# Kernel optimization log

Hardware: AMD Instinct MI355X
Metric: run time of the kernel (lower is better)

Reference implementation:

```python
import jax, jax.numpy as jnp
from jax import lax
import numpy as np

B, T, N, D = 16, 2048, 8, 512


def _div_term(d):
    # exp(arange(0,d,2) * -(ln 10000)/d), as in FixedEmbedding
    return jnp.exp(jnp.arange(0, d, 2).astype(jnp.float32) * (-np.log(10000.0) / d))


def _fixed_table(c, d):
    pos = jnp.arange(c, dtype=jnp.float32)[:, None]
    ang = pos * _div_term(d)  # [c, d/2]
    tab = jnp.zeros((c, d), dtype=jnp.float32)
    tab = tab.at[:, 0::2].set(jnp.sin(ang)).at[:, 1::2].set(jnp.cos(ang))
    return tab


def setup_inputs() -> dict:
    key = jax.random.key(0)
    k1, k2, k3 = jax.random.split(key, 3)
    x = jax.random.normal(k1, (B, T, N), dtype=jnp.float32)
    x_mark = jax.random.randint(k2, (B, T, 4), 0, 7).astype(jnp.int64)
    conv_w = jax.random.normal(k3, (D, N, 3), dtype=jnp.float32) * 0.05
    return {"x": x, "x_mark": x_mark, "conv_w": conv_w}


def reference(x, x_mark, conv_w):
    b, t, n = x.shape
    d = conv_w.shape[0]

    # --- TokenEmbedding: Conv1d(c_in->d_model, k=3, circular padding, no bias) ---
    xp = jnp.transpose(x, (0, 2, 1))  # [b, n, t]
    xpad = jnp.concatenate([xp[..., -1:], xp, xp[..., :1]], axis=-1)  # circular pad 1
    val = lax.conv_general_dilated(
        xpad, conv_w, window_strides=(1,), padding="VALID",
        dimension_numbers=("NCH", "OIH", "NCH"))  # [b, d, t]
    val = jnp.transpose(val, (0, 2, 1))  # [b, t, d]

    # --- TemporalEmbedding (fixed sinusoidal tables), freq='h' ---
    # columns: 0=month(<13), 1=day(<32), 2=weekday(<7), 3=hour(<24)
    temp = (_fixed_table(24, d)[x_mark[:, :, 3]]
            + _fixed_table(7, d)[x_mark[:, :, 2]]
            + _fixed_table(32, d)[x_mark[:, :, 1]]
            + _fixed_table(13, d)[x_mark[:, :, 0]])  # [b, t, d]

    # --- Cycle_PositionalEmbedding (k=1) ---
    fft_abs = jnp.abs(jnp.fft.rfft(x, axis=1))  # [b, t//2+1, n]
    top_idx = jnp.argmax(fft_abs, axis=1)  # [b, n]; topk(k=1) == argmax (first max)
    freqs = jnp.fft.fftfreq(t, d=1.0)  # length t; rfft indices are in range
    periods = jnp.clip(t / freqs[top_idx], 1.0, float(t))  # [b, n]; 0-freq -> inf -> t
    time_idx = jnp.arange(t, dtype=jnp.float32)[None, :, None]  # [1, t, 1]
    pidx = jnp.floor(time_idx % periods[:, None, :])  # [b, t, n] (.long() truncation)

    # FixedEmbedding row for index p is sin/cos(p*div) independent of c_in
    ang = pidx[..., None] * _div_term(d)  # [b, t, n, d/2]
    pe = jnp.stack([jnp.sin(ang), jnp.cos(ang)], axis=-1).reshape(b, t, n, d)
    cyc = pe.mean(axis=2)  # [b, t, d]

    # dropout is identity in eval mode
    return val + temp + cyc
```

## Files before the change

### kernel.cpp

```cpp
#include <hip/hip_runtime.h>
#include <math.h>

#define B_ 16
#define T_ 2048
#define N_ 8
#define D_ 512
#define DTW 4
#define LPAD 520

#define NEG_W0 (-3.0679615757712823e-3f)
#define NEG_W32 (-0.19634954084936207f)
#define NEG_W1024 (-6.1359231515425647e-3f)
#define NEG_LDIV (-0.035977892078031555f)

typedef __attribute__((ext_vector_type(8))) short bf16x8;
typedef __attribute__((ext_vector_type(4))) float f32x4;

static __device__ __forceinline__ short f2bf(float f) {
  unsigned int u = __float_as_uint(f);
  unsigned int r = u + 0x7FFFu + ((u >> 16) & 1u);
  return (short)(r >> 16);
}


__global__ __launch_bounds__(512) void prep_kernel(
    const float* __restrict__ x, const int* __restrict__ xmark,
    const float* __restrict__ convw, float* __restrict__ pmax,
    float* __restrict__ nyqS, float* __restrict__ tab,
    short* __restrict__ amat, short* __restrict__ xbf,
    short* __restrict__ cnt) {
  int tid = threadIdx.x;
  int blk = blockIdx.x;

  if (blk >= 512) {
    int j = blk - 512;
    if (j < 64) {
      int r = j * 512 + tid;
      const float4* xr = (const float4*)(x + (size_t)r * 8);
      float4 lo = xr[0], hi = xr[1];
      bf16x8 v;
      v[0] = f2bf(lo.x); v[1] = f2bf(lo.y); v[2] = f2bf(lo.z); v[3] = f2bf(lo.w);
      v[4] = f2bf(hi.x); v[5] = f2bf(hi.y); v[6] = f2bf(hi.z); v[7] = f2bf(hi.w);
      *(bf16x8*)(xbf + (size_t)r * 8) = v;
      int4 mk = *(const int4*)(xmark + (size_t)r * 4);
      bf16x8 cv;
#pragma unroll
      for (int p = 0; p < 8; ++p) {
        int cc = (mk.x == p) + (mk.y == p) + (mk.z == p) + (mk.w == p);
        cv[p] = f2bf((float)cc);
      }
      *(bf16x8*)(cnt + (size_t)r * 8) = cv;
    } else if (j == 64) {
      int d = tid;
      short row[32];
#pragma unroll
      for (int kk = 0; kk < 24; ++kk) {
        int g = kk >> 3, n = kk & 7;
        row[kk] = f2bf(convw[d * 24 + n * 3 + g]);
      }
      float divv = expf((float)(d >> 1) * NEG_LDIV);
      float s1, c1;
      sincosf(divv, &s1, &c1);
      int odd = d & 1;
      row[24] = f2bf(odd ? 1.f : 0.f);
      float ps = s1, pc = c1;
      row[25] = f2bf(odd ? pc : ps);
#pragma unroll
      for (int p = 2; p < 7; ++p) {
        float ns = fmaf(ps, c1, pc * s1);
        float nc = fmaf(pc, c1, -ps * s1);
        ps = ns; pc = nc;
        row[24 + p] = f2bf(odd ? pc : ps);
      }
      row[31] = 0;
#pragma unroll
      for (int q = 0; q < 4; ++q)
        *(bf16x8*)(amat + d * 32 + q * 8) = *(bf16x8*)&row[q * 8];
    } else {
      int gt = (j - 65) * 512 + tid;
      int tb = gt >> 7;
      int d4 = gt & 127;
      float dv0 = expf((float)(d4 * 2) * NEG_LDIV);
      float dv1 = expf((float)(d4 * 2 + 1) * NEG_LDIV);
      float tf = (float)(tb * 16);
      float s0, c0, s1, c1, r0s, r0c, r1s, r1c;
      sincosf(tf * dv0, &s0, &c0);
      sincosf(tf * dv1, &s1, &c1);
      sincosf(dv0, &r0s, &r0c);
      sincosf(dv1, &r1s, &r1c);
      float* row = tab + (size_t)(tb * 16) * D_ + d4 * 4;
#pragma unroll
      for (int u = 0; u < 16; ++u) {
        f32x4 v; v[0] = s0; v[1] = c0; v[2] = s1; v[3] = c1;
        *(f32x4*)row = v;
        row += D_;
        float ns0 = fmaf(s0, r0c, c0 * r0s), nc0 = fmaf(c0, r0c, -s0 * r0s);
        s0 = ns0; c0 = nc0;
        float ns1 = fmaf(s1, r1c, c1 * r1s), nc1 = fmaf(c1, r1c, -s1 * r1s);
        s1 = ns1; c1 = nc1;
      }
    }
    return;
  }

  __shared__ __align__(16) float2 ybuf[1024];
  __shared__ __align__(16) float2 Bl[1024];
  __shared__ __align__(16) float2 part[512];
  __shared__ float swav[8];
  __shared__ float pwav[4];
  int bn = blk >> 2;
  int parity = (blk >> 1) & 1;
  int h = blk & 1;
  int b = bn >> 3, n = bn & 7;
  const float* xb = x + (size_t)b * (T_ * N_) + n;

  float v0 = xb[tid * 8];
  float v1 = xb[(tid + 512) * 8];
  float v2 = xb[(tid + 1024) * 8];
  float v3 = xb[(tid + 1536) * 8];
  float ea = v0 + v2, eb = v1 + v3;
  float sgn = (tid & 1) ? -(ea + eb) : (ea + eb);
#pragma unroll
  for (int off = 32; off > 0; off >>= 1) sgn += __shfl_down(sgn, off);
  if ((tid & 63) == 0) swav[tid >> 6] = sgn;

  if (parity == 0) {
    float* ya = (float*)ybuf;
    ya[tid] = ea;
    ya[tid + 512] = eb;
  } else {
    float oa = v0 - v2, ob = v1 - v3;
    float ca, sa, cb, sb;
    sincosf((float)tid * NEG_W0, &sa, &ca);
    sincosf((float)(tid + 512) * NEG_W0, &sb, &cb);
    ybuf[tid] = make_float2(oa * ca, oa * sa);
    ybuf[tid + 512] = make_float2(ob * cb, ob * sb);
  }
  __syncthreads();

  int m0 = tid & 31, t0a = tid >> 5;
  float d1 = (float)m0 * NEG_W32;
  float K1 = 2.0f * cosf(d1);
  float c = 1.f, s = 0.f, cp, sp;
  sincosf(-d1, &sp, &cp);
  float ar0 = 0.f, ai0 = 0.f, ar1 = 0.f, ai1 = 0.f;
  if (parity == 0) {
    const float* ya = (const float*)ybuf;
#pragma unroll 8
    for (int t1 = 0; t1 < 32; ++t1) {
      float y0 = ya[t1 * 32 + t0a];
      float y1 = ya[t1 * 32 + t0a + 16];
      ar0 = fmaf(y0, c, ar0); ai0 = fmaf(y0, s, ai0);
      ar1 = fmaf(y1, c, ar1); ai1 = fmaf(y1, s, ai1);
      float nc = fmaf(K1, c, -cp), ns = fmaf(K1, s, -sp);
      cp = c; sp = s; c = nc; s = ns;
    }
  } else {
#pragma unroll 8
    for (int t1 = 0; t1 < 32; ++t1) {
      float2 y0 = ybuf[t1 * 32 + t0a];
      float2 y1 = ybuf[t1 * 32 + t0a + 16];
      ar0 = fmaf(y0.x, c, fmaf(-y0.y, s, ar0));
      ai0 = fmaf(y0.x, s, fmaf(y0.y, c, ai0));
      ar1 = fmaf(y1.x, c, fmaf(-y1.y, s, ar1));
      ai1 = fmaf(y1.x, s, fmaf(y1.y, c, ai1));
      float nc = fmaf(K1, c, -cp), ns = fmaf(K1, s, -sp);
      cp = c; sp = s; c = nc; s = ns;
    }
  }
  {
    float ct, st;
    sincosf((float)(t0a * m0) * NEG_W1024, &st, &ct);
    Bl[t0a * 32 + m0] =
        make_float2(ar0 * ct - ai0 * st, fmaf(ar0, st, ai0 * ct));
    sincosf((float)((t0a + 16) * m0) * NEG_W1024, &st, &ct);
    Bl[(t0a + 16) * 32 + m0] =
        make_float2(ar1 * ct - ai1 * st, fmaf(ar1, st, ai1 * ct));
  }
  __syncthreads();

  int m02 = tid & 31;
  int m1 = h * 8 + ((tid >> 5) & 7);
  int th = tid >> 8;
  float d2 = (float)m1 * NEG_W32;
  float K2 = 2.0f * cosf(d2);
  int t0s = th * 16;
  float c2, s2, c2p, s2p;
  sincosf((float)t0s * d2, &s2, &c2);
  sincosf((float)(t0s - 1) * d2, &s2p, &c2p);
  float yr = 0.f, yi = 0.f;
#pragma unroll 8
  for (int jj = 0; jj < 16; ++jj) {
    float2 bv = Bl[(t0s + jj) * 32 + m02];
    yr = fmaf(bv.x, c2, fmaf(-bv.y, s2, yr));
    yi = fmaf(bv.x, s2, fmaf(bv.y, c2, yi));
    float nc = fmaf(K2, c2, -c2p), ns = fmaf(K2, s2, -s2p);
    c2p = c2; s2p = s2; c2 = nc; s2 = ns;
  }
  part[tid] = make_float2(yr, yi);
  __syncthreads();
  if (tid < 256) {
    float2 pa = part[tid], pb = part[tid + 256];
    float rr = pa.x + pb.x, ii = pa.y + pb.y;
    float P = fmaf(rr, rr, ii * ii);
#pragma unroll
    for (int off = 32; off > 0; off >>= 1) P = fmaxf(P, __shfl_down(P, off));
    if ((tid & 63) == 0) pwav[tid >> 6] = P;
  }
  __syncthreads();
  if (tid < 64) {
    float mxv = (tid < 4) ? pwav[tid] : 0.f;
    float svv = (tid < 8) ? swav[tid] : 0.f;
#pragma unroll
    for (int off = 4; off > 0; off >>= 1) {
      mxv = fmaxf(mxv, __shfl_down(mxv, off));
      svv += __shfl_down(svv, off);
    }
    if (tid == 0) {
      pmax[blk] = mxv;
      if (parity == 0) nyqS[bn] = svv;
    }
  }
}

__global__ __launch_bounds__(512, 4) void main_kernel(
    const short* __restrict__ amat, const short* __restrict__ xbf,
    const short* __restrict__ cnt, const float* __restrict__ tab,
    const float* __restrict__ pmax, const float* __restrict__ nyqS,
    float* __restrict__ out) {
  __shared__ __align__(16) float lds[16 * LPAD];
  int tid = threadIdx.x;
  int lane = tid & 63;
  int w = tid >> 6;
  int c = lane & 15;
  int g = lane >> 4;
  int blk = blockIdx.x;
  int ttile = blk >> 2;
  int bg = blk & 3;
  int t0 = ttile * 16;

  float w1v[4], w0v[4];
#pragma unroll
  for (int j = 0; j < 4; ++j) {
    int b = bg * 4 + j;
    int m = 0;
#pragma unroll
    for (int nn = 0; nn < 8; ++nn) {
      int bn = b * 8 + nn;
      float mx = fmaxf(fmaxf(pmax[4 * bn], pmax[4 * bn + 1]),
                       fmaxf(pmax[4 * bn + 2], pmax[4 * bn + 3]));
      float S = nyqS[bn];
      if (S * S > mx) ++m;
    }
    w1v[j] = (float)(8 - m) * 0.125f;
    w0v[j] = (float)m * 0.125f;
  }

  bf16x8 afrag[DTW];
  f32x4 fet[DTW];
#pragma unroll
  for (int q = 0; q < DTW; ++q) {
    int d0 = (w * DTW + q) * 16;
    afrag[q] = *(const bf16x8*)(amat + (size_t)(d0 + c) * 32 + g * 8);
    fet[q] = *(const f32x4*)(tab + (size_t)(t0 + c) * D_ + d0 + g * 4);
  }

  const f32x4 zac = {0.f, 0.f, 0.f, 0.f};
#pragma unroll
  for (int j = 0; j < 4; ++j) {
    int b = bg * 4 + j;
    bf16x8 bfrag;
    if (g < 3) {
      int row = (t0 + c + g - 1) & (T_ - 1);
      bfrag = *(const bf16x8*)(xbf + ((size_t)b * T_ + row) * 8);
    } else {
      bfrag = *(const bf16x8*)(cnt + ((size_t)b * T_ + t0 + c) * 8);
    }
    float w1 = w1v[j], w0 = w0v[j];
#pragma unroll
    for (int q = 0; q < DTW; ++q) {
      f32x4 acc = __builtin_amdgcn_mfma_f32_16x16x32_bf16(
          afrag[q], bfrag, zac, 0, 0, 0);
      f32x4 ov;
      ov[0] = fmaf(w1, fet[q][0], acc[0]);
      ov[1] = fmaf(w1, fet[q][1], acc[1]) + w0;
      ov[2] = fmaf(w1, fet[q][2], acc[2]);
      ov[3] = fmaf(w1, fet[q][3], acc[3]) + w0;
      int d0 = (w * DTW + q) * 16;
      *(f32x4*)(lds + c * LPAD + d0 + g * 4) = ov;
    }
    __syncthreads();
    float* obase = out + ((size_t)b * T_ + t0) * D_;
#pragma unroll
    for (int r = 0; r < 4; ++r) {
      int e = r * 2048 + tid * 4;
      int trow = e >> 9, col = e & 511;
      f32x4 v = *(const f32x4*)(lds + trow * LPAD + col);
      *(f32x4*)(obase + e) = v;
    }
    __syncthreads();
  }
}

extern "C" void kernel_launch(void* const* d_in, const int* in_sizes, int n_in,
                              void* d_out, int out_size, void* d_ws, size_t ws_size,
                              hipStream_t stream) {
  const float* x = (const float*)d_in[0];
  const int* xmark = (const int*)d_in[1];
  const float* convw = (const float*)d_in[2];
  float* out = (float*)d_out;

  char* ws = (char*)d_ws;
  float* pmax = (float*)ws;
  float* nyqS = pmax + 512;
  float* tab = (float*)(ws + 4096);
  short* amat = (short*)(ws + 4096 + 4194304);
  short* xbf = (short*)(ws + 4096 + 4194304 + 32768);
  short* cnt = (short*)(ws + 4096 + 4194304 + 32768 + 524288);

  prep_kernel<<<609, 512, 0, stream>>>(x, xmark, convw, pmax, nyqS, tab,
                                       amat, xbf, cnt);
  main_kernel<<<(T_ / 16) * (B_ / 4), 512, 0, stream>>>(amat, xbf, cnt, tab,
                                                        pmax, nyqS, out);
}
```

Baseline: 29.83 us.

## Overlap FFT period detection with main GEMM and apply rare correction in fixup kernel

Moves the FFT argmax work into the same launch as the MFMA output kernel, so the output tiles no longer wait on pmax/nyqS. The main path now assumes every channel's period is non-degenerate (weight 1 on the sinusoid table). A new fixup kernel rereads and rewrites output only for batches where some channels hit the Nyquist/zero case. The positional table is now computed directly with one sincos per element instead of rotation recurrences, and the prep kernel is reorganized into 1024-thread blocks. The cost is an extra launch, and for affected batches the output is read and written a second time.

New measurement: 39.89 us. 33.7% more time.

```diff
diff --git a/kernel.cpp b/kernel.cpp
--- a/kernel.cpp
+++ b/kernel.cpp
@@ -23,34 +23,32 @@
 }
 
 
-__global__ __launch_bounds__(512) void prep_kernel(
+__global__ __launch_bounds__(1024) void prep_tail_kernel(
     const float* __restrict__ x, const int* __restrict__ xmark,
-    const float* __restrict__ convw, float* __restrict__ pmax,
-    float* __restrict__ nyqS, float* __restrict__ tab,
+    const float* __restrict__ convw, float* __restrict__ tab,
     short* __restrict__ amat, short* __restrict__ xbf,
     short* __restrict__ cnt) {
   int tid = threadIdx.x;
-  int blk = blockIdx.x;
-
-  if (blk >= 512) {
-    int j = blk - 512;
-    if (j < 64) {
-      int r = j * 512 + tid;
-      const float4* xr = (const float4*)(x + (size_t)r * 8);
-      float4 lo = xr[0], hi = xr[1];
-      bf16x8 v;
-      v[0] = f2bf(lo.x); v[1] = f2bf(lo.y); v[2] = f2bf(lo.z); v[3] = f2bf(lo.w);
-      v[4] = f2bf(hi.x); v[5] = f2bf(hi.y); v[6] = f2bf(hi.z); v[7] = f2bf(hi.w);
-      *(bf16x8*)(xbf + (size_t)r * 8) = v;
-      int4 mk = *(const int4*)(xmark + (size_t)r * 4);
-      bf16x8 cv;
-#pragma unroll
-      for (int p = 0; p < 8; ++p) {
-        int cc = (mk.x == p) + (mk.y == p) + (mk.z == p) + (mk.w == p);
-        cv[p] = f2bf((float)cc);
-      }
-      *(bf16x8*)(cnt + (size_t)r * 8) = cv;
-    } else if (j == 64) {
+  int j = blockIdx.x;
+  if (j < 128) {
+    int base = j * 2048 + tid * 2;
+#pragma unroll
+    for (int u = 0; u < 2; ++u) {
+      int idx = base + u;
+      int t = idx >> 7;
+      int d4 = idx & 127;
+      float ft = (float)t;
+      float dv0 = expf((float)(d4 * 2) * NEG_LDIV);
+      float dv1 = expf((float)(d4 * 2 + 1) * NEG_LDIV);
+      f32x4 v;
+      float s0, c0, s1, c1;
+      sincosf(ft * dv0, &s0, &c0);
+      sincosf(ft * dv1, &s1, &c1);
+      v[0] = s0; v[1] = c0; v[2] = s1; v[3] = c1;
+      *(f32x4*)(tab + (size_t)idx * 4) = v;
+    }
+  } else if (j == 128) {
+    if (tid < 512) {
       int d = tid;
       short row[32];
 #pragma unroll
@@ -76,185 +74,166 @@
 #pragma unroll
       for (int q = 0; q < 4; ++q)
         *(bf16x8*)(amat + d * 32 + q * 8) = *(bf16x8*)&row[q * 8];
+    }
+  } else {
+    int r = (j - 129) * 1024 + tid;
+    const float4* xr = (const float4*)(x + (size_t)r * 8);
+    float4 lo = xr[0], hi = xr[1];
+    bf16x8 v;
+    v[0] = f2bf(lo.x); v[1] = f2bf(lo.y); v[2] = f2bf(lo.z); v[3] = f2bf(lo.w);
+    v[4] = f2bf(hi.x); v[5] = f2bf(hi.y); v[6] = f2bf(hi.z); v[7] = f2bf(hi.w);
+    *(bf16x8*)(xbf + (size_t)r * 8) = v;
+    int4 mk = *(const int4*)(xmark + (size_t)r * 4);
+    bf16x8 cv;
+#pragma unroll
+    for (int p = 0; p < 8; ++p) {
+      int cc = (mk.x == p) + (mk.y == p) + (mk.z == p) + (mk.w == p);
+      cv[p] = f2bf((float)cc);
+    }
+    *(bf16x8*)(cnt + (size_t)r * 8) = cv;
+  }
+}
+
+__global__ __launch_bounds__(512, 6) void fused_kernel(
+    const float* __restrict__ x, const short* __restrict__ amat,
+    const short* __restrict__ xbf, const short* __restrict__ cnt,
+    const float* __restrict__ tab, float* __restrict__ pmax,
+    float* __restrict__ nyqS, float* __restrict__ out) {
+  __shared__ __align__(16) float smem[16 * LPAD];
+  int tid = threadIdx.x;
+  int blk = blockIdx.x;
+
+  if (blk < 512) {
+    float2* ybuf = (float2*)smem;
+    float2* Bl = (float2*)(smem + 2048);
+    float2* part = (float2*)(smem + 4096);
+    float* swav = smem + 5120;
+    float* pwav = smem + 5128;
+    int bn = blk >> 2;
+    int parity = (blk >> 1) & 1;
+    int h = blk & 1;
+    int b = bn >> 3, n = bn & 7;
+    const float* xb = x + (size_t)b * (T_ * N_) + n;
+
+    float v0 = xb[tid * 8];
+    float v1 = xb[(tid + 512) * 8];
+    float v2 = xb[(tid + 1024) * 8];
+    float v3 = xb[(tid + 1536) * 8];
+    float ea = v0 + v2, eb = v1 + v3;
+    float sgn = (tid & 1) ? -(ea + eb) : (ea + eb);
+#pragma unroll
+    for (int off = 32; off > 0; off >>= 1) sgn += __shfl_down(sgn, off);
+    if ((tid & 63) == 0) swav[tid >> 6] = sgn;
+
+    if (parity == 0) {
+      float* ya = (float*)ybuf;
+      ya[tid] = ea;
+      ya[tid + 512] = eb;
     } else {
-      int gt = (j - 65) * 512 + tid;
-      int tb = gt >> 7;
-      int d4 = gt & 127;
-      float dv0 = expf((float)(d4 * 2) * NEG_LDIV);
-      float dv1 = expf((float)(d4 * 2 + 1) * NEG_LDIV);
-      float tf = (float)(tb * 16);
-      float s0, c0, s1, c1, r0s, r0c, r1s, r1c;
-      sincosf(tf * dv0, &s0, &c0);
-      sincosf(tf * dv1, &s1, &c1);
-      sincosf(dv0, &r0s, &r0c);
-      sincosf(dv1, &r1s, &r1c);
-      float* row = tab + (size_t)(tb * 16) * D_ + d4 * 4;
-#pragma unroll
-      for (int u = 0; u < 16; ++u) {
-        f32x4 v; v[0] = s0; v[1] = c0; v[2] = s1; v[3] = c1;
-        *(f32x4*)row = v;
-        row += D_;
-        float ns0 = fmaf(s0, r0c, c0 * r0s), nc0 = fmaf(c0, r0c, -s0 * r0s);
-        s0 = ns0; c0 = nc0;
-        float ns1 = fmaf(s1, r1c, c1 * r1s), nc1 = fmaf(c1, r1c, -s1 * r1s);
-        s1 = ns1; c1 = nc1;
+      float oa = v0 - v2, ob = v1 - v3;
+      float ca, sa, cb, sb;
+      sincosf((float)tid * NEG_W0, &sa, &ca);
+      sincosf((float)(tid + 512) * NEG_W0, &sb, &cb);
+      ybuf[tid] = make_float2(oa * ca, oa * sa);
+      ybuf[tid + 512] = make_float2(ob * cb, ob * sb);
+    }
+    __syncthreads();
+
+    int m0 = tid & 31, t0a = tid >> 5;
+    float d1 = (float)m0 * NEG_W32;
+    float K1 = 2.0f * cosf(d1);
+    float c = 1.f, s = 0.f, cp, sp;
+    sincosf(-d1, &sp, &cp);
+    float ar0 = 0.f, ai0 = 0.f, ar1 = 0.f, ai1 = 0.f;
+    if (parity == 0) {
+      const float* ya = (const float*)ybuf;
+#pragma unroll 8
+      for (int t1 = 0; t1 < 32; ++t1) {
+        float y0 = ya[t1 * 32 + t0a];
+        float y1 = ya[t1 * 32 + t0a + 16];
+        ar0 = fmaf(y0, c, ar0); ai0 = fmaf(y0, s, ai0);
+        ar1 = fmaf(y1, c, ar1); ai1 = fmaf(y1, s, ai1);
+        float nc = fmaf(K1, c, -cp), ns = fmaf(K1, s, -sp);
+        cp = c; sp = s; c = nc; s = ns;
+      }
+    } else {
+#pragma unroll 8
+      for (int t1 = 0; t1 < 32; ++t1) {
+        float2 y0 = ybuf[t1 * 32 + t0a];
+        float2 y1 = ybuf[t1 * 32 + t0a + 16];
+        ar0 = fmaf(y0.x, c, fmaf(-y0.y, s, ar0));
+        ai0 = fmaf(y0.x, s, fmaf(y0.y, c, ai0));
+        ar1 = fmaf(y1.x, c, fmaf(-y1.y, s, ar1));
+        ai1 = fmaf(y1.x, s, fmaf(y1.y, c, ai1));
+        float nc = fmaf(K1, c, -cp), ns = fmaf(K1, s, -sp);
+        cp = c; sp = s; c = nc; s = ns;
+      }
+    }
+    {
+      float ct, st;
+      sincosf((float)(t0a * m0) * NEG_W1024, &st, &ct);
+      Bl[t0a * 32 + m0] =
+          make_float2(ar0 * ct - ai0 * st, fmaf(ar0, st, ai0 * ct));
+      sincosf((float)((t0a + 16) * m0) * NEG_W1024, &st, &ct);
+      Bl[(t0a + 16) * 32 + m0] =
+          make_float2(ar1 * ct - ai1 * st, fmaf(ar1, st, ai1 * ct));
+    }
+    __syncthreads();
+
+    int m02 = tid & 31;
+    int m1 = h * 8 + ((tid >> 5) & 7);
+    int th = tid >> 8;
+    float d2 = (float)m1 * NEG_W32;
+    float K2 = 2.0f * cosf(d2);
+    int t0s = th * 16;
+    float c2, s2, c2p, s2p;
+    sincosf((float)t0s * d2, &s2, &c2);
+    sincosf((float)(t0s - 1) * d2, &s2p, &c2p);
+    float yr = 0.f, yi = 0.f;
+#pragma unroll 8
+    for (int jj = 0; jj < 16; ++jj) {
+      float2 bv = Bl[(t0s + jj) * 32 + m02];
+      yr = fmaf(bv.x, c2, fmaf(-bv.y, s2, yr));
+      yi = fmaf(bv.x, s2, fmaf(bv.y, c2, yi));
+      float nc = fmaf(K2, c2, -c2p), ns = fmaf(K2, s2, -s2p);
+      c2p = c2; s2p = s2; c2 = nc; s2 = ns;
+    }
+    part[tid] = make_float2(yr, yi);
+    __syncthreads();
+    if (tid < 256) {
+      float2 pa = part[tid], pb = part[tid + 256];
+      float rr = pa.x + pb.x, ii = pa.y + pb.y;
+      float P = fmaf(rr, rr, ii * ii);
+#pragma unroll
+      for (int off = 32; off > 0; off >>= 1) P = fmaxf(P, __shfl_down(P, off));
+      if ((tid & 63) == 0) pwav[tid >> 6] = P;
+    }
+    __syncthreads();
+    if (tid < 64) {
+      float mxv = (tid < 4) ? pwav[tid] : 0.f;
+      float svv = (tid < 8) ? swav[tid] : 0.f;
+#pragma unroll
+      for (int off = 4; off > 0; off >>= 1) {
+        mxv = fmaxf(mxv, __shfl_down(mxv, off));
+        svv += __shfl_down(svv, off);
+      }
+      if (tid == 0) {
+        pmax[blk] = mxv;
+        if (parity == 0) nyqS[bn] = svv;
       }
     }
     return;
   }
 
-  __shared__ __align__(16) float2 ybuf[1024];
-  __shared__ __align__(16) float2 Bl[1024];
-  __shared__ __align__(16) float2 part[512];
-  __shared__ float swav[8];
-  __shared__ float pwav[4];
-  int bn = blk >> 2;
-  int parity = (blk >> 1) & 1;
-  int h = blk & 1;
-  int b = bn >> 3, n = bn & 7;
-  const float* xb = x + (size_t)b * (T_ * N_) + n;
-
-  float v0 = xb[tid * 8];
-  float v1 = xb[(tid + 512) * 8];
-  float v2 = xb[(tid + 1024) * 8];
-  float v3 = xb[(tid + 1536) * 8];
-  float ea = v0 + v2, eb = v1 + v3;
-  float sgn = (tid & 1) ? -(ea + eb) : (ea + eb);
-#pragma unroll
-  for (int off = 32; off > 0; off >>= 1) sgn += __shfl_down(sgn, off);
-  if ((tid & 63) == 0) swav[tid >> 6] = sgn;
-
-  if (parity == 0) {
-    float* ya = (float*)ybuf;
-    ya[tid] = ea;
-    ya[tid + 512] = eb;
-  } else {
-    float oa = v0 - v2, ob = v1 - v3;
-    float ca, sa, cb, sb;
-    sincosf((float)tid * NEG_W0, &sa, &ca);
-    sincosf((float)(tid + 512) * NEG_W0, &sb, &cb);
-    ybuf[tid] = make_float2(oa * ca, oa * sa);
-    ybuf[tid + 512] = make_float2(ob * cb, ob * sb);
-  }
-  __syncthreads();
-
-  int m0 = tid & 31, t0a = tid >> 5;
-  float d1 = (float)m0 * NEG_W32;
-  float K1 = 2.0f * cosf(d1);
-  float c = 1.f, s = 0.f, cp, sp;
-  sincosf(-d1, &sp, &cp);
-  float ar0 = 0.f, ai0 = 0.f, ar1 = 0.f, ai1 = 0.f;
-  if (parity == 0) {
-    const float* ya = (const float*)ybuf;
-#pragma unroll 8
-    for (int t1 = 0; t1 < 32; ++t1) {
-      float y0 = ya[t1 * 32 + t0a];
-      float y1 = ya[t1 * 32 + t0a + 16];
-      ar0 = fmaf(y0, c, ar0); ai0 = fmaf(y0, s, ai0);
-      ar1 = fmaf(y1, c, ar1); ai1 = fmaf(y1, s, ai1);
-      float nc = fmaf(K1, c, -cp), ns = fmaf(K1, s, -sp);
-      cp = c; sp = s; c = nc; s = ns;
-    }
-  } else {
-#pragma unroll 8
-    for (int t1 = 0; t1 < 32; ++t1) {
-      float2 y0 = ybuf[t1 * 32 + t0a];
-      float2 y1 = ybuf[t1 * 32 + t0a + 16];
-      ar0 = fmaf(y0.x, c, fmaf(-y0.y, s, ar0));
-      ai0 = fmaf(y0.x, s, fmaf(y0.y, c, ai0));
-      ar1 = fmaf(y1.x, c, fmaf(-y1.y, s, ar1));
-      ai1 = fmaf(y1.x, s, fmaf(y1.y, c, ai1));
-      float nc = fmaf(K1, c, -cp), ns = fmaf(K1, s, -sp);
-      cp = c; sp = s; c = nc; s = ns;
-    }
-  }
-  {
-    float ct, st;
-    sincosf((float)(t0a * m0) * NEG_W1024, &st, &ct);
-    Bl[t0a * 32 + m0] =
-        make_float2(ar0 * ct - ai0 * st, fmaf(ar0, st, ai0 * ct));
-    sincosf((float)((t0a + 16) * m0) * NEG_W1024, &st, &ct);
-    Bl[(t0a + 16) * 32 + m0] =
-        make_float2(ar1 * ct - ai1 * st, fmaf(ar1, st, ai1 * ct));
-  }
-  __syncthreads();
-
-  int m02 = tid & 31;
-  int m1 = h * 8 + ((tid >> 5) & 7);
-  int th = tid >> 8;
-  float d2 = (float)m1 * NEG_W32;
-  float K2 = 2.0f * cosf(d2);
-  int t0s = th * 16;
-  float c2, s2, c2p, s2p;
-  sincosf((float)t0s * d2, &s2, &c2);
-  sincosf((float)(t0s - 1) * d2, &s2p, &c2p);
-  float yr = 0.f, yi = 0.f;
-#pragma unroll 8
-  for (int jj = 0; jj < 16; ++jj) {
-    float2 bv = Bl[(t0s + jj) * 32 + m02];
-    yr = fmaf(bv.x, c2, fmaf(-bv.y, s2, yr));
-    yi = fmaf(bv.x, s2, fmaf(bv.y, c2, yi));
-    float nc = fmaf(K2, c2, -c2p), ns = fmaf(K2, s2, -s2p);
-    c2p = c2; s2p = s2; c2 = nc; s2 = ns;
-  }
-  part[tid] = make_float2(yr, yi);
-  __syncthreads();
-  if (tid < 256) {
-    float2 pa = part[tid], pb = part[tid + 256];
-    float rr = pa.x + pb.x, ii = pa.y + pb.y;
-    float P = fmaf(rr, rr, ii * ii);
-#pragma unroll
-    for (int off = 32; off > 0; off >>= 1) P = fmaxf(P, __shfl_down(P, off));
-    if ((tid & 63) == 0) pwav[tid >> 6] = P;
-  }
-  __syncthreads();
-  if (tid < 64) {
-    float mxv = (tid < 4) ? pwav[tid] : 0.f;
-    float svv = (tid < 8) ? swav[tid] : 0.f;
-#pragma unroll
-    for (int off = 4; off > 0; off >>= 1) {
-      mxv = fmaxf(mxv, __shfl_down(mxv, off));
-      svv += __shfl_down(svv, off);
-    }
-    if (tid == 0) {
-      pmax[blk] = mxv;
-      if (parity == 0) nyqS[bn] = svv;
-    }
-  }
-}
-
-__global__ __launch_bounds__(512, 4) void main_kernel(
-    const short* __restrict__ amat, const short* __restrict__ xbf,
-    const short* __restrict__ cnt, const float* __restrict__ tab,
-    const float* __restrict__ pmax, const float* __restrict__ nyqS,
-    float* __restrict__ out) {
-  __shared__ __align__(16) float lds[16 * LPAD];
-  int tid = threadIdx.x;
+  float* lds = smem;
   int lane = tid & 63;
   int w = tid >> 6;
   int c = lane & 15;
   int g = lane >> 4;
-  int blk = blockIdx.x;
-  int ttile = blk >> 2;
-  int bg = blk & 3;
+  int inner = blk - 512;
+  int ttile = inner & 127;
+  int bg = inner >> 7;
   int t0 = ttile * 16;
-
-  float w1v[4], w0v[4];
-#pragma unroll
-  for (int j = 0; j < 4; ++j) {
-    int b = bg * 4 + j;
-    int m = 0;
-#pragma unroll
-    for (int nn = 0; nn < 8; ++nn) {
-      int bn = b * 8 + nn;
-      float mx = fmaxf(fmaxf(pmax[4 * bn], pmax[4 * bn + 1]),
-                       fmaxf(pmax[4 * bn + 2], pmax[4 * bn + 3]));
-      float S = nyqS[bn];
-      if (S * S > mx) ++m;
-    }
-    w1v[j] = (float)(8 - m) * 0.125f;
-    w0v[j] = (float)m * 0.125f;
-  }
 
   bf16x8 afrag[DTW];
   f32x4 fet[DTW];
@@ -267,8 +246,8 @@
 
   const f32x4 zac = {0.f, 0.f, 0.f, 0.f};
 #pragma unroll
-  for (int j = 0; j < 4; ++j) {
-    int b = bg * 4 + j;
+  for (int j = 0; j < 2; ++j) {
+    int b = bg * 2 + j;
     bf16x8 bfrag;
     if (g < 3) {
       int row = (t0 + c + g - 1) & (T_ - 1);
@@ -276,16 +255,15 @@
     } else {
       bfrag = *(const bf16x8*)(cnt + ((size_t)b * T_ + t0 + c) * 8);
     }
-    float w1 = w1v[j], w0 = w0v[j];
 #pragma unroll
     for (int q = 0; q < DTW; ++q) {
       f32x4 acc = __builtin_amdgcn_mfma_f32_16x16x32_bf16(
           afrag[q], bfrag, zac, 0, 0, 0);
       f32x4 ov;
-      ov[0] = fmaf(w1, fet[q][0], acc[0]);
-      ov[1] = fmaf(w1, fet[q][1], acc[1]) + w0;
-      ov[2] = fmaf(w1, fet[q][2], acc[2]);
-      ov[3] = fmaf(w1, fet[q][3], acc[3]) + w0;
+      ov[0] = acc[0] + fet[q][0];
+      ov[1] = acc[1] + fet[q][1];
+      ov[2] = acc[2] + fet[q][2];
+      ov[3] = acc[3] + fet[q][3];
       int d0 = (w * DTW + q) * 16;
       *(f32x4*)(lds + c * LPAD + d0 + g * 4) = ov;
     }
@@ -298,7 +276,40 @@
       f32x4 v = *(const f32x4*)(lds + trow * LPAD + col);
       *(f32x4*)(obase + e) = v;
     }
-    __syncthreads();
+    if (j == 0) __syncthreads();
+  }
+}
+
+__global__ __launch_bounds__(1024) void fixup_kernel(
+    const float* __restrict__ pmax, const float* __restrict__ nyqS,
+    const float* __restrict__ tab, float* __restrict__ out) {
+  int j = blockIdx.x;
+  int b = j >> 4;
+  int chunk = j & 15;
+  int m = 0;
+#pragma unroll
+  for (int nn = 0; nn < 8; ++nn) {
+    int bn = b * 8 + nn;
+    float mx = fmaxf(fmaxf(pmax[4 * bn], pmax[4 * bn + 1]),
+                     fmaxf(pmax[4 * bn + 2], pmax[4 * bn + 3]));
+    float S = nyqS[bn];
+    if (S * S > mx) ++m;
+  }
+  if (m == 0) return;
+  float wm = -(float)m * 0.125f;
+  float w0 = (float)m * 0.125f;
+  size_t obase = ((size_t)b * T_ + chunk * 128) * D_;
+  size_t tbase = (size_t)(chunk * 128) * D_;
+#pragma unroll
+  for (int r = 0; r < 16; ++r) {
+    size_t off = (size_t)(r * 1024 + threadIdx.x) * 4;
+    f32x4 ov = *(f32x4*)(out + obase + off);
+    f32x4 tv = *(const f32x4*)(tab + tbase + off);
+    ov[0] = fmaf(wm, tv[0], ov[0]);
+    ov[1] = fmaf(wm, tv[1], ov[1]) + w0;
+    ov[2] = fmaf(wm, tv[2], ov[2]);
+    ov[3] = fmaf(wm, tv[3], ov[3]) + w0;
+    *(f32x4*)(out + obase + off) = ov;
   }
 }
 
@@ -318,8 +329,9 @@
   short* xbf = (short*)(ws + 4096 + 4194304 + 32768);
   short* cnt = (short*)(ws + 4096 + 4194304 + 32768 + 524288);
 
-  prep_kernel<<<609, 512, 0, stream>>>(x, xmark, convw, pmax, nyqS, tab,
-                                       amat, xbf, cnt);
-  main_kernel<<<(T_ / 16) * (B_ / 4), 512, 0, stream>>>(amat, xbf, cnt, tab,
-                                                        pmax, nyqS, out);
-}
+  prep_tail_kernel<<<161, 1024, 0, stream>>>(x, xmark, convw, tab, amat,
+                                             xbf, cnt);
+  fused_kernel<<<1536, 512, 0, stream>>>(x, amat, xbf, cnt, tab, pmax, nyqS,
+                                         out);
+  fixup_kernel<<<256, 1024, 0, stream>>>(pmax, nyqS, tab, out);
+}
```
